# Optimization experiments

Hardware: AMD Instinct MI355X
Metric: run time of the kernel (lower is better)

Reference implementation:

```python
import jax, jax.numpy as jnp
import numpy as np

B, T, N_EMBED, HEAD_SIZE = 512, 256, 384, 64

def setup_inputs() -> dict:
    key = jax.random.key(0)
    k1, k2, k3, k4 = jax.random.split(key, 4)
    x = jax.random.normal(k1, (B, T, N_EMBED), dtype=jnp.float32)
    # nn.Linear(n_embed, head_size, bias=False) weights, stored as [in, out] for x @ W
    scale = 1.0 / np.sqrt(N_EMBED)
    Wk = jax.random.uniform(k2, (N_EMBED, HEAD_SIZE), jnp.float32, -scale, scale)
    Wq = jax.random.uniform(k3, (N_EMBED, HEAD_SIZE), jnp.float32, -scale, scale)
    Wv = jax.random.uniform(k4, (N_EMBED, HEAD_SIZE), jnp.float32, -scale, scale)
    return {"x": x, "Wk": Wk, "Wq": Wq, "Wv": Wv}

def reference(x, Wk, Wq, Wv):
    # Single causal self-attention head (dropout in eval mode / identity)
    k = x @ Wk  # [B, T, H]
    q = x @ Wq
    v = x @ Wv
    wei = jnp.einsum('bth,bsh->bts', q, k) * (HEAD_SIZE ** -0.5)  # [B, T, T]
    causal = jnp.tril(jnp.ones((T, T), dtype=bool))
    wei = jnp.where(causal, wei, -jnp.inf)
    wei = jax.nn.softmax(wei, axis=-1)
    out = jnp.einsum('bts,bsh->bth', wei, v)  # [B, T, H]
    return out
```

## Files before the change

kernel.cpp:

```cpp
#include <hip/hip_runtime.h>
#include <stdint.h>


typedef short s16x8 __attribute__((ext_vector_type(8)));
typedef short s16x4 __attribute__((ext_vector_type(4)));
typedef float f32x4 __attribute__((ext_vector_type(4)));

#define LOG2E_OVER_8 0.18033688011112042f

__device__ inline short f2bf(float f) {
  union { float f; uint32_t u; } v; v.f = f;
  uint32_t r = (v.u + 0x7fffu + ((v.u >> 16) & 1u)) >> 16;
  return (short)r;
}

__global__ __launch_bounds__(256) void prep_w(const float* __restrict__ Wk,
                                              const float* __restrict__ Wq,
                                              const float* __restrict__ Wv,
                                              short* __restrict__ Wt3) {
  int idx = blockIdx.x * 256 + threadIdx.x;
  int j = idx & 7;
  int lane = (idx >> 3) & 63;
  int rest = idx >> 9;
  int ntile = rest % 12;
  int kc = rest / 12;
  int n = ntile * 16 + (lane & 15);
  int kk = (lane >> 4) * 8 + j;
  int col = n & 63;
  int w = n >> 6;
  const float* W = (w == 0) ? Wk : (w == 1) ? Wq : Wv;
  float v = W[(kc * 32 + kk) * 64 + col];
  if (w == 1) v *= LOG2E_OVER_8;
  Wt3[idx] = f2bf(v);
}

__global__ __launch_bounds__(1024) void fused_head(const float* __restrict__ x,
                                                   const short* __restrict__ Wt3,
                                                   float* __restrict__ out) {
  __shared__ __align__(16) short LDS[81920];
  short* Kf = LDS;
  short* Qf = LDS + 16384;
  short* Vf = LDS + 32768;
  short* Pb = LDS + 49152;
  short* Xc = LDS + 49152;
  short* Wsl = LDS + 49152 + 8192;

  const int tid = threadIdx.x;
  const int wave = tid >> 6;
  const int lane = tid & 63;
  const int l15 = lane & 15;
  const int quad = lane >> 4;
  const int b = blockIdx.x;
  const float* xb = x + (long)b * (256 * 384);

  const int mgrp = wave >> 2;
  const int ngrp = wave & 3;

  const int m0s = tid >> 3;
  const int kq0 = (tid & 7) * 4;
  const int xoff0 = m0s * 384 + kq0;
  const int xoff1 = xoff0 + 128 * 384;
  const int lds0 = (m0s >> 4) * 512 + ((m0s & 15) + (kq0 >> 3) * 16) * 8 + (kq0 & 7);
  const int lds1 = lds0 + 8 * 512;
  const bool wact = (tid < 768);

  f32x4 acc[4][3];
#pragma unroll
  for (int i = 0; i < 4; ++i)
#pragma unroll
    for (int k2 = 0; k2 < 3; ++k2) acc[i][k2] = (f32x4)0.0f;

  f32x4 xa0 = *(const f32x4*)(xb + xoff0);
  f32x4 xa1 = *(const f32x4*)(xb + xoff1);
  s16x8 wv;
  if (wact) wv = *(const s16x8*)(Wt3 + tid * 8);

  for (int kc = 0; kc < 12; ++kc) {
    __syncthreads();
    s16x4 h0, h1;
    h0[0] = f2bf(xa0[0]); h0[1] = f2bf(xa0[1]); h0[2] = f2bf(xa0[2]); h0[3] = f2bf(xa0[3]);
    h1[0] = f2bf(xa1[0]); h1[1] = f2bf(xa1[1]); h1[2] = f2bf(xa1[2]); h1[3] = f2bf(xa1[3]);
    *(s16x4*)(Xc + lds0) = h0;
    *(s16x4*)(Xc + lds1) = h1;
    if (wact) *(s16x8*)(Wsl + tid * 8) = wv;
    __syncthreads();
    if (kc < 11) {
      xa0 = *(const f32x4*)(xb + xoff0 + (kc + 1) * 32);
      xa1 = *(const f32x4*)(xb + xoff1 + (kc + 1) * 32);
      if (wact) wv = *(const s16x8*)(Wt3 + (kc + 1) * 6144 + tid * 8);
    }
    s16x8 af[4];
#pragma unroll
    for (int i = 0; i < 4; ++i)
      af[i] = *(const s16x8*)(Xc + (mgrp * 4 + i) * 512 + lane * 8);
#pragma unroll
    for (int k2 = 0; k2 < 3; ++k2) {
      s16x8 bfv = *(const s16x8*)(Wsl + (ngrp * 3 + k2) * 512 + lane * 8);
#pragma unroll
      for (int i = 0; i < 4; ++i)
        acc[i][k2] = __builtin_amdgcn_mfma_f32_16x16x32_bf16(af[i], bfv, acc[i][k2], 0, 0, 0);
    }
  }

#pragma unroll
  for (int i = 0; i < 4; ++i) {
    const int rowb = (mgrp * 4 + i) * 16 + quad * 4;
#pragma unroll
    for (int k2 = 0; k2 < 3; ++k2) {
      const int nt = ngrp * 3 + k2;
      const int h = (nt * 16 + l15) & 63;
      const int which = nt >> 2;
#pragma unroll
      for (int r = 0; r < 4; ++r) {
        const short v = f2bf(acc[i][k2][r]);
        const int row = rowb + r;
        if (which == 0)
          Kf[((row >> 4) * 2 + (h >> 5)) * 512 + ((row & 15) + ((h & 31) >> 3) * 16) * 8 + (h & 7)] = v;
        else if (which == 1)
          Qf[((row >> 4) * 2 + (h >> 5)) * 512 + ((row & 15) + ((h & 31) >> 3) * 16) * 8 + (h & 7)] = v;
        else
          Vf[((row >> 5) * 4 + (h >> 4)) * 512 + ((h & 15) + ((row & 31) >> 3) * 16) * 8 + (row & 7)] = v;
      }
    }
  }
  __syncthreads();

  const int t = wave;
  const int q0 = t * 16;
  short* Pw = Pb + wave * 2048;

  s16x8 qf0 = *(const s16x8*)(Qf + (t * 2 + 0) * 512 + lane * 8);
  s16x8 qf1 = *(const s16x8*)(Qf + (t * 2 + 1) * 512 + lane * 8);

  f32x4 Oacc[4];
#pragma unroll
  for (int n = 0; n < 4; ++n) Oacc[n] = (f32x4)0.0f;
  float mrow[4] = {-1e30f, -1e30f, -1e30f, -1e30f};
  float lrow[4] = {0.f, 0.f, 0.f, 0.f};

  const int nb = (t >= 8) ? 2 : 1;
  for (int cb = 0; cb < nb; ++cb) {
    const int st0 = cb * 8;
    const bool last = (cb == nb - 1);
    const int nuse = last ? (t - cb * 8 + 1) : 8;

    float S[8][4];
#pragma unroll
    for (int n = 0; n < 8; ++n) {
      if (n < nuse) {
        s16x8 kf0 = *(const s16x8*)(Kf + ((st0 + n) * 2 + 0) * 512 + lane * 8);
        s16x8 kf1 = *(const s16x8*)(Kf + ((st0 + n) * 2 + 1) * 512 + lane * 8);
        f32x4 z = (f32x4)0.0f;
        z = __builtin_amdgcn_mfma_f32_16x16x32_bf16(qf0, kf0, z, 0, 0, 0);
        z = __builtin_amdgcn_mfma_f32_16x16x32_bf16(qf1, kf1, z, 0, 0, 0);
        if (last) {
          const int s_abs = cb * 128 + n * 16 + l15;
#pragma unroll
          for (int r = 0; r < 4; ++r) {
            const int q_abs = q0 + quad * 4 + r;
            S[n][r] = (s_abs > q_abs) ? -1e30f : z[r];
          }
        } else {
#pragma unroll
          for (int r = 0; r < 4; ++r) S[n][r] = z[r];
        }
      } else {
#pragma unroll
        for (int r = 0; r < 4; ++r) S[n][r] = -1e30f;
      }
    }

    float alpha[4];
#pragma unroll
    for (int r = 0; r < 4; ++r) {
      float mx = S[0][r];
#pragma unroll
      for (int n = 1; n < 8; ++n) mx = fmaxf(mx, S[n][r]);
      mx = fmaxf(mx, __shfl_xor(mx, 1));
      mx = fmaxf(mx, __shfl_xor(mx, 2));
      mx = fmaxf(mx, __shfl_xor(mx, 4));
      mx = fmaxf(mx, __shfl_xor(mx, 8));
      float mnew = fmaxf(mrow[r], mx);
      alpha[r] = __builtin_amdgcn_exp2f(mrow[r] - mnew);
      mrow[r] = mnew;
    }
    float rs[4] = {0.f, 0.f, 0.f, 0.f};
#pragma unroll
    for (int n = 0; n < 8; ++n) {
#pragma unroll
      for (int r = 0; r < 4; ++r) {
        float p = __builtin_amdgcn_exp2f(S[n][r] - mrow[r]);
        rs[r] += p;
        Pw[(n >> 1) * 512 + ((quad * 4 + r) + ((n & 1) * 2 + (l15 >> 3)) * 16) * 8 + (l15 & 7)] = f2bf(p);
      }
    }
#pragma unroll
    for (int r = 0; r < 4; ++r) {
      float s = rs[r];
      s += __shfl_xor(s, 1);
      s += __shfl_xor(s, 2);
      s += __shfl_xor(s, 4);
      s += __shfl_xor(s, 8);
      lrow[r] = lrow[r] * alpha[r] + s;
#pragma unroll
      for (int n = 0; n < 4; ++n) Oacc[n][r] *= alpha[r];
    }
    asm volatile("s_waitcnt lgkmcnt(0)" ::: "memory");

    const int kblks = (nuse + 1) >> 1;
    for (int sb = 0; sb < kblks; ++sb) {
      s16x8 pf = *(const s16x8*)(Pw + sb * 512 + lane * 8);
#pragma unroll
      for (int n2 = 0; n2 < 4; ++n2) {
        s16x8 vfv = *(const s16x8*)(Vf + ((cb * 4 + sb) * 4 + n2) * 512 + lane * 8);
        Oacc[n2] = __builtin_amdgcn_mfma_f32_16x16x32_bf16(pf, vfv, Oacc[n2], 0, 0, 0);
      }
    }
  }

  float inv[4];
#pragma unroll
  for (int r = 0; r < 4; ++r) inv[r] = 1.0f / lrow[r];
  float* ob = out + ((long)b * 256 + q0 + quad * 4) * 64;
#pragma unroll
  for (int n = 0; n < 4; ++n)
#pragma unroll
    for (int r = 0; r < 4; ++r)
      ob[r * 64 + n * 16 + l15] = Oacc[n][r] * inv[r];
}

extern "C" void kernel_launch(void* const* d_in, const int* in_sizes, int n_in,
                              void* d_out, int out_size, void* d_ws, size_t ws_size,
                              hipStream_t stream) {
  const float* x = (const float*)d_in[0];
  const float* Wk = (const float*)d_in[1];
  const float* Wq = (const float*)d_in[2];
  const float* Wv = (const float*)d_in[3];
  float* out = (float*)d_out;
  short* Wt3 = (short*)d_ws;

  prep_w<<<288, 256, 0, stream>>>(Wk, Wq, Wv, Wt3);
  fused_head<<<512, 1024, 0, stream>>>(x, Wt3, out);
}
```

Before: 318.5 us.

## Split fused head into separate QKV projection and attention kernels via global workspace

Replaces the single 1024-thread fused kernel with two 256-thread kernels. The first projects 64-row slices of x into bf16 K/Q/V tiles stored in global workspace, holding weights in registers and double-buffering x in LDS. The second runs attention with four query tiles per block, interleaved for causal load balance, and reads K/V straight from global memory. The aim is higher occupancy and more blocks than the old one-block-per-batch design with its large LDS footprint, at the cost of an extra round trip of K/Q/V through global memory and a third launch.

```diff
diff --git a/kernel.cpp b/kernel.cpp
--- a/kernel.cpp
+++ b/kernel.cpp
@@ -3,7 +3,6 @@
 
 
 typedef short s16x8 __attribute__((ext_vector_type(8)));
-typedef short s16x4 __attribute__((ext_vector_type(4)));
 typedef float f32x4 __attribute__((ext_vector_type(4)));
 
 #define LOG2E_OVER_8 0.18033688011112042f
@@ -34,103 +33,121 @@
   Wt3[idx] = f2bf(v);
 }
 
-__global__ __launch_bounds__(1024) void fused_head(const float* __restrict__ x,
-                                                   const short* __restrict__ Wt3,
-                                                   float* __restrict__ out) {
-  __shared__ __align__(16) short LDS[81920];
-  short* Kf = LDS;
-  short* Qf = LDS + 16384;
-  short* Vf = LDS + 32768;
-  short* Pb = LDS + 49152;
-  short* Xc = LDS + 49152;
-  short* Wsl = LDS + 49152 + 8192;
-
+__global__ __launch_bounds__(256, 4) void qkv(const float* __restrict__ x,
+                                              const short* __restrict__ Wt3,
+                                              short* __restrict__ Kd,
+                                              short* __restrict__ Qd,
+                                              short* __restrict__ Vd) {
+  __shared__ __align__(16) short Xbuf[2][2048];
+  __shared__ __align__(16) short Rb[12288];
   const int tid = threadIdx.x;
   const int wave = tid >> 6;
   const int lane = tid & 63;
   const int l15 = lane & 15;
   const int quad = lane >> 4;
-  const int b = blockIdx.x;
-  const float* xb = x + (long)b * (256 * 384);
-
-  const int mgrp = wave >> 2;
-  const int ngrp = wave & 3;
-
-  const int m0s = tid >> 3;
-  const int kq0 = (tid & 7) * 4;
-  const int xoff0 = m0s * 384 + kq0;
-  const int xoff1 = xoff0 + 128 * 384;
-  const int lds0 = (m0s >> 4) * 512 + ((m0s & 15) + (kq0 >> 3) * 16) * 8 + (kq0 & 7);
-  const int lds1 = lds0 + 8 * 512;
-  const bool wact = (tid < 768);
+  const int b = blockIdx.x >> 2;
+  const int rb = blockIdx.x & 3;
+  const float* xb = x + ((long)b * 256 + rb * 64) * 384;
+
+  const int row = tid >> 2;
+  const int c8 = (tid & 3) * 8;
+  const float* xp = xb + row * 384 + c8;
+  const int xwoff = (row >> 4) * 512 + ((row & 15) + (c8 >> 3) * 16) * 8;
+  const short* wp = Wt3 + (wave * 3) * 512 + lane * 8;
 
   f32x4 acc[4][3];
 #pragma unroll
-  for (int i = 0; i < 4; ++i)
-#pragma unroll
-    for (int k2 = 0; k2 < 3; ++k2) acc[i][k2] = (f32x4)0.0f;
-
-  f32x4 xa0 = *(const f32x4*)(xb + xoff0);
-  f32x4 xa1 = *(const f32x4*)(xb + xoff1);
-  s16x8 wv;
-  if (wact) wv = *(const s16x8*)(Wt3 + tid * 8);
-
+  for (int mt = 0; mt < 4; ++mt)
+#pragma unroll
+    for (int lnt = 0; lnt < 3; ++lnt) acc[mt][lnt] = (f32x4)0.0f;
+
+  f32x4 xa[2][2];
+  s16x8 wv[2][3];
+  xa[0][0] = *(const f32x4*)xp;
+  xa[0][1] = *(const f32x4*)(xp + 4);
+#pragma unroll
+  for (int lnt = 0; lnt < 3; ++lnt) wv[0][lnt] = *(const s16x8*)(wp + lnt * 512);
+
+#pragma unroll
   for (int kc = 0; kc < 12; ++kc) {
-    __syncthreads();
-    s16x4 h0, h1;
-    h0[0] = f2bf(xa0[0]); h0[1] = f2bf(xa0[1]); h0[2] = f2bf(xa0[2]); h0[3] = f2bf(xa0[3]);
-    h1[0] = f2bf(xa1[0]); h1[1] = f2bf(xa1[1]); h1[2] = f2bf(xa1[2]); h1[3] = f2bf(xa1[3]);
-    *(s16x4*)(Xc + lds0) = h0;
-    *(s16x4*)(Xc + lds1) = h1;
-    if (wact) *(s16x8*)(Wsl + tid * 8) = wv;
+    const int cur = kc & 1, nxt = cur ^ 1;
+    s16x8 hv;
+    hv[0] = f2bf(xa[cur][0][0]); hv[1] = f2bf(xa[cur][0][1]);
+    hv[2] = f2bf(xa[cur][0][2]); hv[3] = f2bf(xa[cur][0][3]);
+    hv[4] = f2bf(xa[cur][1][0]); hv[5] = f2bf(xa[cur][1][1]);
+    hv[6] = f2bf(xa[cur][1][2]); hv[7] = f2bf(xa[cur][1][3]);
+    *(s16x8*)(&Xbuf[cur][0] + xwoff) = hv;
     __syncthreads();
     if (kc < 11) {
-      xa0 = *(const f32x4*)(xb + xoff0 + (kc + 1) * 32);
-      xa1 = *(const f32x4*)(xb + xoff1 + (kc + 1) * 32);
-      if (wact) wv = *(const s16x8*)(Wt3 + (kc + 1) * 6144 + tid * 8);
+      xa[nxt][0] = *(const f32x4*)(xp + (kc + 1) * 32);
+      xa[nxt][1] = *(const f32x4*)(xp + (kc + 1) * 32 + 4);
+#pragma unroll
+      for (int lnt = 0; lnt < 3; ++lnt)
+        wv[nxt][lnt] = *(const s16x8*)(wp + (kc + 1) * 6144 + lnt * 512);
     }
     s16x8 af[4];
 #pragma unroll
-    for (int i = 0; i < 4; ++i)
-      af[i] = *(const s16x8*)(Xc + (mgrp * 4 + i) * 512 + lane * 8);
-#pragma unroll
-    for (int k2 = 0; k2 < 3; ++k2) {
-      s16x8 bfv = *(const s16x8*)(Wsl + (ngrp * 3 + k2) * 512 + lane * 8);
-#pragma unroll
-      for (int i = 0; i < 4; ++i)
-        acc[i][k2] = __builtin_amdgcn_mfma_f32_16x16x32_bf16(af[i], bfv, acc[i][k2], 0, 0, 0);
-    }
-  }
-
-#pragma unroll
-  for (int i = 0; i < 4; ++i) {
-    const int rowb = (mgrp * 4 + i) * 16 + quad * 4;
-#pragma unroll
-    for (int k2 = 0; k2 < 3; ++k2) {
-      const int nt = ngrp * 3 + k2;
-      const int h = (nt * 16 + l15) & 63;
-      const int which = nt >> 2;
+    for (int mt = 0; mt < 4; ++mt)
+      af[mt] = *(const s16x8*)(&Xbuf[cur][0] + mt * 512 + lane * 8);
+#pragma unroll
+    for (int lnt = 0; lnt < 3; ++lnt)
+#pragma unroll
+      for (int mt = 0; mt < 4; ++mt)
+        acc[mt][lnt] = __builtin_amdgcn_mfma_f32_16x16x32_bf16(af[mt], wv[cur][lnt], acc[mt][lnt], 0, 0, 0);
+  }
+
+#pragma unroll
+  for (int mt = 0; mt < 4; ++mt) {
+#pragma unroll
+    for (int lnt = 0; lnt < 3; ++lnt) {
+      const int ntg = wave * 3 + lnt;
 #pragma unroll
       for (int r = 0; r < 4; ++r) {
-        const short v = f2bf(acc[i][k2][r]);
-        const int row = rowb + r;
-        if (which == 0)
-          Kf[((row >> 4) * 2 + (h >> 5)) * 512 + ((row & 15) + ((h & 31) >> 3) * 16) * 8 + (h & 7)] = v;
-        else if (which == 1)
-          Qf[((row >> 4) * 2 + (h >> 5)) * 512 + ((row & 15) + ((h & 31) >> 3) * 16) * 8 + (h & 7)] = v;
-        else
-          Vf[((row >> 5) * 4 + (h >> 4)) * 512 + ((h & 15) + ((row & 31) >> 3) * 16) * 8 + (row & 7)] = v;
+        const short v = f2bf(acc[mt][lnt][r]);
+        if (ntg < 8) {
+          const int h = (ntg & 3) * 16 + l15;
+          const int base = (ntg < 4) ? 0 : 4096;
+          Rb[base + (mt * 2 + (h >> 5)) * 512 + ((quad * 4 + r) + ((h & 31) >> 3) * 16) * 8 + (h & 7)] = v;
+        } else {
+          const int ht = ntg - 8;
+          const int rr = mt * 16 + quad * 4 + r;
+          Rb[8192 + ((rr >> 5) * 4 + ht) * 512 + (l15 + ((rr & 31) >> 3) * 16) * 8 + (rr & 7)] = v;
+        }
       }
     }
   }
   __syncthreads();
 
-  const int t = wave;
+  const long Kbase = ((long)b * 16 + rb * 4) * 1024;
+  const long Vbase = ((long)b * 8 + rb * 2) * 2048;
+#pragma unroll
+  for (int i = 0; i < 6; ++i) {
+    const int s = (tid + i * 256) * 8;
+    s16x8 vdat = *(const s16x8*)&Rb[s];
+    if (i < 2)      *(s16x8*)(Kd + Kbase + s) = vdat;
+    else if (i < 4) *(s16x8*)(Qd + Kbase + (s - 4096)) = vdat;
+    else            *(s16x8*)(Vd + Vbase + (s - 8192)) = vdat;
+  }
+}
+
+__global__ __launch_bounds__(256, 5) void attn(const short* __restrict__ Kd,
+                                               const short* __restrict__ Qd,
+                                               const short* __restrict__ Vd,
+                                               float* __restrict__ out) {
+  __shared__ __align__(16) short P[4][1024];
+  const int tid = threadIdx.x;
+  const int wave = tid >> 6;
+  const int lane = tid & 63;
+  const int l15 = lane & 15;
+  const int quad = lane >> 4;
+  const int b = blockIdx.x >> 2;
+  const int qt = blockIdx.x & 3;
+  const int t = qt + wave * 4;
   const int q0 = t * 16;
-  short* Pw = Pb + wave * 2048;
-
-  s16x8 qf0 = *(const s16x8*)(Qf + (t * 2 + 0) * 512 + lane * 8);
-  s16x8 qf1 = *(const s16x8*)(Qf + (t * 2 + 1) * 512 + lane * 8);
+  short* Pw = &P[wave][0];
+
+  s16x8 qf0 = *(const s16x8*)(Qd + (((long)b * 16 + t) * 2 + 0) * 512 + lane * 8);
+  s16x8 qf1 = *(const s16x8*)(Qd + (((long)b * 16 + t) * 2 + 1) * 512 + lane * 8);
 
   f32x4 Oacc[4];
 #pragma unroll
@@ -138,28 +155,32 @@
   float mrow[4] = {-1e30f, -1e30f, -1e30f, -1e30f};
   float lrow[4] = {0.f, 0.f, 0.f, 0.f};
 
-  const int nb = (t >= 8) ? 2 : 1;
-  for (int cb = 0; cb < nb; ++cb) {
-    const int st0 = cb * 8;
-    const bool last = (cb == nb - 1);
-    const int nuse = last ? (t - cb * 8 + 1) : 8;
-
-    float S[8][4];
-#pragma unroll
-    for (int n = 0; n < 8; ++n) {
+  const int nch = (t >> 2) + 1;
+  for (int c = 0; c < nch; ++c) {
+    const int st0 = c * 4;
+    const int nuse = min(4, t - st0 + 1);
+
+    s16x8 kf0[4], kf1[4];
+#pragma unroll
+    for (int n = 0; n < 4; ++n) {
       if (n < nuse) {
-        s16x8 kf0 = *(const s16x8*)(Kf + ((st0 + n) * 2 + 0) * 512 + lane * 8);
-        s16x8 kf1 = *(const s16x8*)(Kf + ((st0 + n) * 2 + 1) * 512 + lane * 8);
+        const long kb = (((long)b * 16 + st0 + n) * 2) * 512 + lane * 8;
+        kf0[n] = *(const s16x8*)(Kd + kb);
+        kf1[n] = *(const s16x8*)(Kd + kb + 512);
+      }
+    }
+    float S[4][4];
+#pragma unroll
+    for (int n = 0; n < 4; ++n) {
+      if (n < nuse) {
         f32x4 z = (f32x4)0.0f;
-        z = __builtin_amdgcn_mfma_f32_16x16x32_bf16(qf0, kf0, z, 0, 0, 0);
-        z = __builtin_amdgcn_mfma_f32_16x16x32_bf16(qf1, kf1, z, 0, 0, 0);
-        if (last) {
-          const int s_abs = cb * 128 + n * 16 + l15;
-#pragma unroll
-          for (int r = 0; r < 4; ++r) {
-            const int q_abs = q0 + quad * 4 + r;
-            S[n][r] = (s_abs > q_abs) ? -1e30f : z[r];
-          }
+        z = __builtin_amdgcn_mfma_f32_16x16x32_bf16(qf0, kf0[n], z, 0, 0, 0);
+        z = __builtin_amdgcn_mfma_f32_16x16x32_bf16(qf1, kf1[n], z, 0, 0, 0);
+        if (st0 + n == t) {
+          const int s_abs = (st0 + n) * 16 + l15;
+#pragma unroll
+          for (int r = 0; r < 4; ++r)
+            S[n][r] = (s_abs > q0 + quad * 4 + r) ? -1e30f : z[r];
         } else {
 #pragma unroll
           for (int r = 0; r < 4; ++r) S[n][r] = z[r];
@@ -173,9 +194,7 @@
     float alpha[4];
 #pragma unroll
     for (int r = 0; r < 4; ++r) {
-      float mx = S[0][r];
-#pragma unroll
-      for (int n = 1; n < 8; ++n) mx = fmaxf(mx, S[n][r]);
+      float mx = fmaxf(fmaxf(S[0][r], S[1][r]), fmaxf(S[2][r], S[3][r]));
       mx = fmaxf(mx, __shfl_xor(mx, 1));
       mx = fmaxf(mx, __shfl_xor(mx, 2));
       mx = fmaxf(mx, __shfl_xor(mx, 4));
@@ -186,7 +205,7 @@
     }
     float rs[4] = {0.f, 0.f, 0.f, 0.f};
 #pragma unroll
-    for (int n = 0; n < 8; ++n) {
+    for (int n = 0; n < 4; ++n) {
 #pragma unroll
       for (int r = 0; r < 4; ++r) {
         float p = __builtin_amdgcn_exp2f(S[n][r] - mrow[r]);
@@ -211,9 +230,9 @@
     for (int sb = 0; sb < kblks; ++sb) {
       s16x8 pf = *(const s16x8*)(Pw + sb * 512 + lane * 8);
 #pragma unroll
-      for (int n2 = 0; n2 < 4; ++n2) {
-        s16x8 vfv = *(const s16x8*)(Vf + ((cb * 4 + sb) * 4 + n2) * 512 + lane * 8);
-        Oacc[n2] = __builtin_amdgcn_mfma_f32_16x16x32_bf16(pf, vfv, Oacc[n2], 0, 0, 0);
+      for (int ht = 0; ht < 4; ++ht) {
+        s16x8 vf = *(const s16x8*)(Vd + (((long)b * 8 + c * 2 + sb) * 4 + ht) * 512 + lane * 8);
+        Oacc[ht] = __builtin_amdgcn_mfma_f32_16x16x32_bf16(pf, vf, Oacc[ht], 0, 0, 0);
       }
     }
   }
@@ -237,8 +256,13 @@
   const float* Wq = (const float*)d_in[2];
   const float* Wv = (const float*)d_in[3];
   float* out = (float*)d_out;
-  short* Wt3 = (short*)d_ws;
+  char* ws = (char*)d_ws;
+  short* Wt3 = (short*)ws;
+  short* Kd = (short*)(ws + 262144);
+  short* Qd = (short*)(ws + 262144 + 16777216);
+  short* Vd = (short*)(ws + 262144 + 2 * 16777216);
 
   prep_w<<<288, 256, 0, stream>>>(Wk, Wq, Wv, Wt3);
-  fused_head<<<512, 1024, 0, stream>>>(x, Wt3, out);
-}
+  qkv<<<2048, 256, 0, stream>>>(x, Wt3, Kd, Qd, Vd);
+  attn<<<2048, 256, 0, stream>>>(Kd, Qd, Vd, out);
+}
```

Measured after the change: 357.9 us. 12.4% more time.
